# Kernel optimization log

Measured on AMD Instinct MI355X. Metric: run time of the kernel, lower is better.

Reference implementation:

```python
import jax, jax.numpy as jnp
import numpy as np

# norse LIFParameters defaults with v_th overridden to 0.23
DT = 1e-3
TAU_SYN_INV = 200.0   # 1/5e-3
TAU_MEM_INV = 100.0   # 1/1e-2
V_TH = 0.23
ENC_V_TH = 1.0        # encoder uses default LIFParameters (v_th=1.0)
SEQ_LEN = 24
HIDDEN = 256
N_CLASSES = 10


def heaviside(x):
    return (x > 0).astype(x.dtype)


def encode(x):
    """ConstantCurrentLIFEncoder: lif_current_encoder over SEQ_LEN steps. x: [B, F] -> [T, B, F] spikes."""
    def step(v, _):
        v = v + DT * TAU_MEM_INV * (x - v)          # dv = dt*tau_mem_inv*((v_leak - v) + I)
        z = heaviside(v - ENC_V_TH)
        v = (1.0 - z) * v                            # reset to v_reset = 0
        return v, z
    _, zs = jax.lax.scan(step, jnp.zeros_like(x), None, length=SEQ_LEN)
    return zs


def lif_ff_step(inp, v, i):
    """norse lif_feed_forward_step: decay v with old i, decay i, spike, reset, then add input to i."""
    v_dec = v + DT * TAU_MEM_INV * (i - v)           # v_leak = 0
    i_dec = i * (1.0 - DT * TAU_SYN_INV)
    z = heaviside(v_dec - V_TH)
    v_new = (1.0 - z) * v_dec                        # v_reset = 0
    i_new = i_dec + inp
    return z, v_new, i_new


def setup_inputs() -> dict:
    key = jax.random.key(0)
    ks = jax.random.split(key, 8)
    B, F = 4096, 1024
    def lin(k, fan_in, fan_out):
        bound = 1.0 / np.sqrt(fan_in)
        kw, kb = jax.random.split(k)
        W = jax.random.uniform(kw, (fan_out, fan_in), jnp.float32, -bound, bound)
        b = jax.random.uniform(kb, (fan_out,), jnp.float32, -bound, bound)
        return W, b
    x = jax.random.normal(ks[0], (B, F), jnp.float32)
    W1, b1 = lin(ks[1], F, HIDDEN)
    W2, b2 = lin(ks[2], HIDDEN, HIDDEN)
    W3, b3 = lin(ks[3], HIDDEN, HIDDEN)
    Wli = jax.random.normal(ks[4], (N_CLASSES, HIDDEN), jnp.float32) * np.sqrt(2.0 / HIDDEN)
    return {"x": x, "W1": W1, "b1": b1, "W2": W2, "b2": b2, "W3": W3, "b3": b3, "Wli": Wli}


def reference(x, W1, b1, W2, b2, W3, b3, Wli):
    # dropout layers are identity in eval mode
    enc = encode(x)                                   # [T, B, F]
    B = x.shape[0]
    z2 = lambda d: jnp.zeros((B, d), x.dtype)
    carry0 = (z2(HIDDEN), z2(HIDDEN), z2(HIDDEN), z2(HIDDEN), z2(HIDDEN), z2(HIDDEN),
              z2(N_CLASSES), z2(N_CLASSES))
    def step(c, z):
        v1, i1, v2, i2, v3, i3, vo, io = c
        o1, v1, i1 = lif_ff_step(z @ W1.T + b1, v1, i1)
        o2, v2, i2 = lif_ff_step(o1 @ W2.T + b2, v2, i2)
        o2 = o2 + o1                                  # residual
        o3, v3, i3 = lif_ff_step(o2 @ W3.T + b3, v3, i3)
        o3 = o3 + o2                                  # residual
        # LILinearCell li_step: v from old i, i decays then accumulates W @ input (no bias)
        vo = vo + DT * TAU_MEM_INV * (io - vo)
        io = io * (1.0 - DT * TAU_SYN_INV) + o3 @ Wli.T
        return (v1, i1, v2, i2, v3, i3, vo, io), vo
    _, voltages = jax.lax.scan(step, carry0, enc)     # [T, B, n_classes]
    return voltages[-1]                               # decode = last timestep
```

## Files before the change

kernel.cpp:

```cpp
#include <hip/hip_runtime.h>
#include <hip/hip_bf16.h>

#define FEAT   1024
#define HID    256
#define TSTEPS 24
#define NCLS   10

typedef unsigned int u32;
typedef unsigned long long u64;

constexpr int OFF_W1T  = 0;
constexpr int OFF_W2T  = OFF_W1T + FEAT*HID;
constexpr int OFF_W3T  = OFF_W2T + HID*HID;
constexpr int OFF_WLI  = OFF_W3T + HID*HID;
constexpr int OFF_B1   = OFF_WLI + NCLS*HID;
constexpr int OFF_B2   = OFF_B1 + HID;
constexpr int OFF_B3   = OFF_B2 + HID;
constexpr int OFF_FLAG = OFF_B3 + HID;

struct CoefT { float c[TSTEPS]; };
constexpr CoefT make_coef() {
    CoefT r{};
    double c = 0.0;
    double p9 = 1.0;
    r.c[TSTEPS-1] = 0.0f;
    for (int u = TSTEPS-1; u > 0; u--) {
        c = 0.8 * c + 0.1 * p9;
        p9 *= 0.9;
        r.c[u-1] = (float)c;
    }
    return r;
}
__device__ constexpr CoefT COEF = make_coef();

__global__ void detect_dtype_k(const void* __restrict__ x, u32* __restrict__ flag) {
    __shared__ int bad;
    if (threadIdx.x == 0) bad = 0;
    __syncthreads();
    float v = __bfloat162float(((const __hip_bfloat16*)x)[threadIdx.x]);
    if (!(fabsf(v) < 100.0f)) atomicOr(&bad, 1);
    __syncthreads();
    if (threadIdx.x == 0) *flag = bad ? 0u : 1u;
}

__device__ __forceinline__ float rd_any(const void* p, int idx, u32 isbf) {
    return isbf ? __bfloat162float(((const __hip_bfloat16*)p)[idx])
                : ((const float*)p)[idx];
}

__global__ void prep_weights_k(const void* W1, const void* W2, const void* W3,
                               const void* Wli, const void* b1, const void* b2,
                               const void* b3, float* __restrict__ ws) {
    const u32 isbf = ((const u32*)(ws + OFF_FLAG))[0];
    int id = blockIdx.x * 256 + threadIdx.x;
    if (id < FEAT*HID) {
        int f = id >> 8, h = id & 255;
        ws[OFF_W1T + id] = rd_any(W1, h*FEAT + f, isbf);
        return;
    }
    id -= FEAT*HID;
    if (id < HID*HID) {
        int f = id >> 8, h = id & 255;
        ws[OFF_W2T + id] = rd_any(W2, h*HID + f, isbf);
        return;
    }
    id -= HID*HID;
    if (id < HID*HID) {
        int f = id >> 8, h = id & 255;
        ws[OFF_W3T + id] = rd_any(W3, h*HID + f, isbf);
        return;
    }
    id -= HID*HID;
    if (id < NCLS*HID) {
        ws[OFF_WLI + id] = rd_any(Wli, id, isbf);
        return;
    }
    id -= NCLS*HID;
    if (id < HID) { ws[OFF_B1 + id] = rd_any(b1, id, isbf); return; }
    id -= HID;
    if (id < HID) { ws[OFF_B2 + id] = rd_any(b2, id, isbf); return; }
    id -= HID;
    if (id < HID) { ws[OFF_B3 + id] = rd_any(b3, id, isbf); return; }
}

__device__ __forceinline__ float bits_as_f32(u32 b) { return __uint_as_float(b); }

__device__ __forceinline__ void add_col(float* acc, const float* __restrict__ Wt,
                                        u32 col, u32 lane4) {
    col = (u32)__builtin_amdgcn_readfirstlane((int)col);
    const float4 w = *(const float4*)(Wt + ((size_t)col << 8) + lane4);
    acc[0] += w.x; acc[1] += w.y; acc[2] += w.z; acc[3] += w.w;
}

template<int ISBF>
__global__ __launch_bounds__(256) void snn_k(const void* __restrict__ xin,
                                             const float* __restrict__ ws,
                                             void* __restrict__ out) {
    const u32 flag = ((const u32*)(ws + OFF_FLAG))[0];
    if (flag != (u32)ISBF) return;

    const u32 tid  = threadIdx.x;
    const u32 lane = tid & 63;
    const u32 wv   = tid >> 6;
    const int row  = blockIdx.x * 4 + wv;
    const u32 lane4 = lane * 4;

    const float* __restrict__ W1T = ws + OFF_W1T;
    const float* __restrict__ W2T = ws + OFF_W2T;
    const float* __restrict__ W3T = ws + OFF_W3T;
    const float* __restrict__ WLI = ws + OFF_WLI;

    u32   xpk[8];
    float xf[16];
    if constexpr (ISBF) {
        const unsigned short* xp = (const unsigned short*)xin + (size_t)row*FEAT;
        #pragma unroll
        for (int j = 0; j < 8; j++) {
            u32 lo = xp[(2*j)*64 + lane];
            u32 hi = xp[(2*j+1)*64 + lane];
            xpk[j] = lo | (hi << 16);
        }
    } else {
        const float* xp = (const float*)xin + (size_t)row*FEAT;
        #pragma unroll
        for (int k = 0; k < 16; k++) xf[k] = xp[k*64 + lane];
    }

    float venc[16];
    #pragma unroll
    for (int k = 0; k < 16; k++) venc[k] = 0.0f;

    float v1[4], i1[4], v2[4], i2[4], v3[4], i3[4], g[4];
    #pragma unroll
    for (int k = 0; k < 4; k++) {
        v1[k]=0.f; i1[k]=0.f; v2[k]=0.f; i2[k]=0.f; v3[k]=0.f; i3[k]=0.f; g[k]=0.f;
    }
    const float4 b1v = *(const float4*)(ws + OFF_B1 + lane4);
    const float4 b2v = *(const float4*)(ws + OFF_B2 + lane4);
    const float4 b3v = *(const float4*)(ws + OFF_B3 + lane4);

    for (int t = 0; t < TSTEPS; t++) {
        float a1[4] = {b1v.x, b1v.y, b1v.z, b1v.w};
        #pragma unroll
        for (int k = 0; k < 16; k++) {
            float xk;
            if constexpr (ISBF)
                xk = (k & 1) ? bits_as_f32(xpk[k>>1] & 0xffff0000u)
                             : bits_as_f32(xpk[k>>1] << 16);
            else
                xk = xf[k];
            float vd = venc[k] + 0.1f * (xk - venc[k]);
            bool z = vd > 1.0f;
            venc[k] = z ? 0.0f : vd;
            u64 m = __ballot(z);
            while (m) {
                u32 p = (u32)__builtin_ctzll(m);
                m &= m - 1;
                add_col(a1, W1T, (u32)(k << 6) | p, lane4);
            }
        }

        float o1v[4]; u64 m1[4];
        #pragma unroll
        for (int kk = 0; kk < 4; kk++) {
            float vd = v1[kk] + 0.1f * (i1[kk] - v1[kk]);
            i1[kk] = i1[kk] * 0.8f;
            bool z = vd > 0.23f;
            v1[kk] = z ? 0.0f : vd;
            i1[kk] = i1[kk] + a1[kk];
            o1v[kk] = z ? 1.0f : 0.0f;
            m1[kk] = __ballot(z);
        }

        float a2[4] = {b2v.x, b2v.y, b2v.z, b2v.w};
        #pragma unroll
        for (int kk = 0; kk < 4; kk++) {
            u64 m = m1[kk];
            while (m) {
                u32 p = (u32)__builtin_ctzll(m);
                m &= m - 1;
                add_col(a2, W2T, (p << 2) | (u32)kk, lane4);
            }
        }

        float o2v[4]; u64 m2[4];
        #pragma unroll
        for (int kk = 0; kk < 4; kk++) {
            float vd = v2[kk] + 0.1f * (i2[kk] - v2[kk]);
            i2[kk] = i2[kk] * 0.8f;
            bool z = vd > 0.23f;
            v2[kk] = z ? 0.0f : vd;
            i2[kk] = i2[kk] + a2[kk];
            o2v[kk] = (z ? 1.0f : 0.0f) + o1v[kk];
            m2[kk] = __ballot(z);
        }

        float a3[4] = {b3v.x, b3v.y, b3v.z, b3v.w};
        #pragma unroll
        for (int kk = 0; kk < 4; kk++) {
            u64 m = m2[kk];
            while (m) {
                u32 p = (u32)__builtin_ctzll(m);
                m &= m - 1;
                add_col(a3, W3T, (p << 2) | (u32)kk, lane4);
            }
        }
        #pragma unroll
        for (int kk = 0; kk < 4; kk++) {
            u64 m = m1[kk];
            while (m) {
                u32 p = (u32)__builtin_ctzll(m);
                m &= m - 1;
                add_col(a3, W3T, (p << 2) | (u32)kk, lane4);
            }
        }

        const float cf = COEF.c[t];
        #pragma unroll
        for (int kk = 0; kk < 4; kk++) {
            float vd = v3[kk] + 0.1f * (i3[kk] - v3[kk]);
            i3[kk] = i3[kk] * 0.8f;
            bool z = vd > 0.23f;
            v3[kk] = z ? 0.0f : vd;
            i3[kk] = i3[kk] + a3[kk];
            float o3 = (z ? 1.0f : 0.0f) + o2v[kk];
            g[kk] += cf * o3;
        }
    }

    float s[NCLS];
    #pragma unroll
    for (int c = 0; c < NCLS; c++) {
        const float4 w = *(const float4*)(WLI + c*HID + lane4);
        float p = g[0]*w.x + g[1]*w.y + g[2]*w.z + g[3]*w.w;
        #pragma unroll
        for (int d = 32; d > 0; d >>= 1) p += __shfl_xor(p, d, 64);
        s[c] = p;
    }
    if (lane == 0) {
        if constexpr (ISBF) {
            __hip_bfloat16* o = (__hip_bfloat16*)out + (size_t)row*NCLS;
            #pragma unroll
            for (int c = 0; c < NCLS; c++) o[c] = __float2bfloat16(s[c]);
        } else {
            float* o = (float*)out + (size_t)row*NCLS;
            #pragma unroll
            for (int c = 0; c < NCLS; c++) o[c] = s[c];
        }
    }
}

extern "C" void kernel_launch(void* const* d_in, const int* in_sizes, int n_in,
                              void* d_out, int out_size, void* d_ws, size_t ws_size,
                              hipStream_t stream) {
    const void* x   = d_in[0];
    const void* W1  = d_in[1];
    const void* b1  = d_in[2];
    const void* W2  = d_in[3];
    const void* b2  = d_in[4];
    const void* W3  = d_in[5];
    const void* b3  = d_in[6];
    const void* Wli = d_in[7];
    float* ws = (float*)d_ws;
    const int batch = in_sizes[0] / FEAT;

    u32* flag = (u32*)(ws + OFF_FLAG);
    detect_dtype_k<<<1, 256, 0, stream>>>(x, flag);

    const int prep_elems = FEAT*HID + HID*HID + HID*HID + NCLS*HID + 3*HID;
    prep_weights_k<<<(prep_elems + 255)/256, 256, 0, stream>>>(W1, W2, W3, Wli, b1, b2, b3, ws);

    const int grid = batch / 4;
    snn_k<1><<<grid, 256, 0, stream>>>(x, ws, d_out);
    snn_k<0><<<grid, 256, 0, stream>>>(x, ws, d_out);
}
```

Before: 166.6 us.

## Batch spike-driven weight gathers four at a time and merge dtype kernel variants

The sparse column-gather loops now pull four set bits per iteration and issue four independent float4 loads into four separate accumulator sets. Missing slots are masked with zero-weight FMAs. This raises memory-level parallelism and breaks the serial add dependency. The weight transpose in prep now reads coalesced and scatters its writes. The two templated dtype kernels are merged into one kernel with a runtime branch, removing one launch. The risks are extra wasted loads when spike counts are low and higher register pressure under launch_bounds(256,4).

New measurement: 439.6 us. 164% more time.

```diff
diff --git a/kernel.cpp b/kernel.cpp
--- a/kernel.cpp
+++ b/kernel.cpp
@@ -21,8 +21,7 @@
 struct CoefT { float c[TSTEPS]; };
 constexpr CoefT make_coef() {
     CoefT r{};
-    double c = 0.0;
-    double p9 = 1.0;
+    double c = 0.0, p9 = 1.0;
     r.c[TSTEPS-1] = 0.0f;
     for (int u = TSTEPS-1; u > 0; u--) {
         c = 0.8 * c + 0.1 * p9;
@@ -54,27 +53,24 @@
     const u32 isbf = ((const u32*)(ws + OFF_FLAG))[0];
     int id = blockIdx.x * 256 + threadIdx.x;
     if (id < FEAT*HID) {
-        int f = id >> 8, h = id & 255;
-        ws[OFF_W1T + id] = rd_any(W1, h*FEAT + f, isbf);
+        int h = id >> 10, f = id & 1023;
+        ws[OFF_W1T + f*HID + h] = rd_any(W1, id, isbf);
         return;
     }
     id -= FEAT*HID;
     if (id < HID*HID) {
-        int f = id >> 8, h = id & 255;
-        ws[OFF_W2T + id] = rd_any(W2, h*HID + f, isbf);
+        int h = id >> 8, f = id & 255;
+        ws[OFF_W2T + f*HID + h] = rd_any(W2, id, isbf);
         return;
     }
     id -= HID*HID;
     if (id < HID*HID) {
-        int f = id >> 8, h = id & 255;
-        ws[OFF_W3T + id] = rd_any(W3, h*HID + f, isbf);
+        int h = id >> 8, f = id & 255;
+        ws[OFF_W3T + f*HID + h] = rd_any(W3, id, isbf);
         return;
     }
     id -= HID*HID;
-    if (id < NCLS*HID) {
-        ws[OFF_WLI + id] = rd_any(Wli, id, isbf);
-        return;
-    }
+    if (id < NCLS*HID) { ws[OFF_WLI + id] = rd_any(Wli, id, isbf); return; }
     id -= NCLS*HID;
     if (id < HID) { ws[OFF_B1 + id] = rd_any(b1, id, isbf); return; }
     id -= HID;
@@ -83,22 +79,51 @@
     if (id < HID) { ws[OFF_B3 + id] = rd_any(b3, id, isbf); return; }
 }
 
-__device__ __forceinline__ float bits_as_f32(u32 b) { return __uint_as_float(b); }
-
-__device__ __forceinline__ void add_col(float* acc, const float* __restrict__ Wt,
-                                        u32 col, u32 lane4) {
-    col = (u32)__builtin_amdgcn_readfirstlane((int)col);
-    const float4 w = *(const float4*)(Wt + ((size_t)col << 8) + lane4);
-    acc[0] += w.x; acc[1] += w.y; acc[2] += w.z; acc[3] += w.w;
-}
-
-template<int ISBF>
-__global__ __launch_bounds__(256) void snn_k(const void* __restrict__ xin,
-                                             const float* __restrict__ ws,
-                                             void* __restrict__ out) {
-    const u32 flag = ((const u32*)(ws + OFF_FLAG))[0];
-    if (flag != (u32)ISBF) return;
-
+struct Acc4 {
+    float q[4][4];
+    __device__ __forceinline__ void init(const float4 b) {
+        q[0][0]=b.x; q[0][1]=b.y; q[0][2]=b.z; q[0][3]=b.w;
+        #pragma unroll
+        for (int j = 1; j < 4; j++)
+            #pragma unroll
+            for (int i = 0; i < 4; i++) q[j][i] = 0.f;
+    }
+    __device__ __forceinline__ void fin(float out[4]) {
+        #pragma unroll
+        for (int i = 0; i < 4; i++) out[i] = (q[0][i]+q[1][i]) + (q[2][i]+q[3][i]);
+    }
+};
+
+template<int CMUL>
+__device__ __forceinline__ void gather4(Acc4& A, const float* __restrict__ Wt,
+                                        u64 m, u32 base, u32 lane4) {
+    const float* __restrict__ Wb = Wt + ((size_t)base << 8) + lane4;
+    while (m) {
+        u32 c0 = (u32)__builtin_ctzll(m); m &= m - 1;
+        bool h1 = m != 0; u32 c1 = h1 ? (u32)__builtin_ctzll(m) : c0; m &= m - 1;
+        bool h2 = m != 0; u32 c2 = h2 ? (u32)__builtin_ctzll(m) : c0; m &= m - 1;
+        bool h3 = m != 0; u32 c3 = h3 ? (u32)__builtin_ctzll(m) : c0; m &= m - 1;
+        const float4 w0 = *(const float4*)(Wb + ((size_t)c0 * CMUL << 8));
+        const float4 w1 = *(const float4*)(Wb + ((size_t)c1 * CMUL << 8));
+        const float4 w2 = *(const float4*)(Wb + ((size_t)c2 * CMUL << 8));
+        const float4 w3 = *(const float4*)(Wb + ((size_t)c3 * CMUL << 8));
+        const float f1 = h1 ? 1.f : 0.f;
+        const float f2 = h2 ? 1.f : 0.f;
+        const float f3 = h3 ? 1.f : 0.f;
+        A.q[0][0] += w0.x; A.q[0][1] += w0.y; A.q[0][2] += w0.z; A.q[0][3] += w0.w;
+        A.q[1][0] = fmaf(f1, w1.x, A.q[1][0]); A.q[1][1] = fmaf(f1, w1.y, A.q[1][1]);
+        A.q[1][2] = fmaf(f1, w1.z, A.q[1][2]); A.q[1][3] = fmaf(f1, w1.w, A.q[1][3]);
+        A.q[2][0] = fmaf(f2, w2.x, A.q[2][0]); A.q[2][1] = fmaf(f2, w2.y, A.q[2][1]);
+        A.q[2][2] = fmaf(f2, w2.z, A.q[2][2]); A.q[2][3] = fmaf(f2, w2.w, A.q[2][3]);
+        A.q[3][0] = fmaf(f3, w3.x, A.q[3][0]); A.q[3][1] = fmaf(f3, w3.y, A.q[3][1]);
+        A.q[3][2] = fmaf(f3, w3.z, A.q[3][2]); A.q[3][3] = fmaf(f3, w3.w, A.q[3][3]);
+    }
+}
+
+__global__ __launch_bounds__(256, 4) void snn_k(const void* __restrict__ xin,
+                                                const float* __restrict__ ws,
+                                                void* __restrict__ out) {
+    const u32 isbf = ((const u32*)(ws + OFF_FLAG))[0];
     const u32 tid  = threadIdx.x;
     const u32 lane = tid & 63;
     const u32 wv   = tid >> 6;
@@ -110,16 +135,11 @@
     const float* __restrict__ W3T = ws + OFF_W3T;
     const float* __restrict__ WLI = ws + OFF_WLI;
 
-    u32   xpk[8];
     float xf[16];
-    if constexpr (ISBF) {
-        const unsigned short* xp = (const unsigned short*)xin + (size_t)row*FEAT;
-        #pragma unroll
-        for (int j = 0; j < 8; j++) {
-            u32 lo = xp[(2*j)*64 + lane];
-            u32 hi = xp[(2*j+1)*64 + lane];
-            xpk[j] = lo | (hi << 16);
-        }
+    if (isbf) {
+        const __hip_bfloat16* xp = (const __hip_bfloat16*)xin + (size_t)row*FEAT;
+        #pragma unroll
+        for (int k = 0; k < 16; k++) xf[k] = __bfloat162float(xp[k*64 + lane]);
     } else {
         const float* xp = (const float*)xin + (size_t)row*FEAT;
         #pragma unroll
@@ -140,25 +160,16 @@
     const float4 b3v = *(const float4*)(ws + OFF_B3 + lane4);
 
     for (int t = 0; t < TSTEPS; t++) {
-        float a1[4] = {b1v.x, b1v.y, b1v.z, b1v.w};
+        Acc4 A1; A1.init(b1v);
         #pragma unroll
         for (int k = 0; k < 16; k++) {
-            float xk;
-            if constexpr (ISBF)
-                xk = (k & 1) ? bits_as_f32(xpk[k>>1] & 0xffff0000u)
-                             : bits_as_f32(xpk[k>>1] << 16);
-            else
-                xk = xf[k];
-            float vd = venc[k] + 0.1f * (xk - venc[k]);
+            float vd = venc[k] + 0.1f * (xf[k] - venc[k]);
             bool z = vd > 1.0f;
             venc[k] = z ? 0.0f : vd;
             u64 m = __ballot(z);
-            while (m) {
-                u32 p = (u32)__builtin_ctzll(m);
-                m &= m - 1;
-                add_col(a1, W1T, (u32)(k << 6) | p, lane4);
-            }
-        }
+            gather4<1>(A1, W1T, m, (u32)(k << 6), lane4);
+        }
+        float a1[4]; A1.fin(a1);
 
         float o1v[4]; u64 m1[4];
         #pragma unroll
@@ -172,16 +183,10 @@
             m1[kk] = __ballot(z);
         }
 
-        float a2[4] = {b2v.x, b2v.y, b2v.z, b2v.w};
-        #pragma unroll
-        for (int kk = 0; kk < 4; kk++) {
-            u64 m = m1[kk];
-            while (m) {
-                u32 p = (u32)__builtin_ctzll(m);
-                m &= m - 1;
-                add_col(a2, W2T, (p << 2) | (u32)kk, lane4);
-            }
-        }
+        Acc4 A2; A2.init(b2v);
+        #pragma unroll
+        for (int kk = 0; kk < 4; kk++) gather4<4>(A2, W2T, m1[kk], (u32)kk, lane4);
+        float a2[4]; A2.fin(a2);
 
         float o2v[4]; u64 m2[4];
         #pragma unroll
@@ -195,25 +200,12 @@
             m2[kk] = __ballot(z);
         }
 
-        float a3[4] = {b3v.x, b3v.y, b3v.z, b3v.w};
-        #pragma unroll
-        for (int kk = 0; kk < 4; kk++) {
-            u64 m = m2[kk];
-            while (m) {
-                u32 p = (u32)__builtin_ctzll(m);
-                m &= m - 1;
-                add_col(a3, W3T, (p << 2) | (u32)kk, lane4);
-            }
-        }
-        #pragma unroll
-        for (int kk = 0; kk < 4; kk++) {
-            u64 m = m1[kk];
-            while (m) {
-                u32 p = (u32)__builtin_ctzll(m);
-                m &= m - 1;
-                add_col(a3, W3T, (p << 2) | (u32)kk, lane4);
-            }
-        }
+        Acc4 A3; A3.init(b3v);
+        #pragma unroll
+        for (int kk = 0; kk < 4; kk++) gather4<4>(A3, W3T, m2[kk], (u32)kk, lane4);
+        #pragma unroll
+        for (int kk = 0; kk < 4; kk++) gather4<4>(A3, W3T, m1[kk], (u32)kk, lane4);
+        float a3[4]; A3.fin(a3);
 
         const float cf = COEF.c[t];
         #pragma unroll
@@ -238,7 +230,7 @@
         s[c] = p;
     }
     if (lane == 0) {
-        if constexpr (ISBF) {
+        if (isbf) {
             __hip_bfloat16* o = (__hip_bfloat16*)out + (size_t)row*NCLS;
             #pragma unroll
             for (int c = 0; c < NCLS; c++) o[c] = __float2bfloat16(s[c]);
@@ -270,7 +262,5 @@
     const int prep_elems = FEAT*HID + HID*HID + HID*HID + NCLS*HID + 3*HID;
     prep_weights_k<<<(prep_elems + 255)/256, 256, 0, stream>>>(W1, W2, W3, Wli, b1, b2, b3, ws);
 
-    const int grid = batch / 4;
-    snn_k<1><<<grid, 256, 0, stream>>>(x, ws, d_out);
-    snn_k<0><<<grid, 256, 0, stream>>>(x, ws, d_out);
-}
+    snn_k<<<batch/4, 256, 0, stream>>>(x, ws, d_out);
+}
```
